# Kernel optimization log

Measured on AMD Instinct MI355X. Metric: run time of the kernel, lower is better.

## Reference

```python
import jax, jax.numpy as jnp
import numpy as np

EPS = 1e-5

def yat_dense(x, kernel, bias, alpha):
    # scaled by (sqrt(F)/log(1+F))**alpha, plus bias.
    y = x @ kernel  # [..., F]
    dist = jnp.sum(x * x, axis=-1, keepdims=True) + jnp.sum(kernel * kernel, axis=0) - 2.0 * y
    out = (y * y) / (dist + EPS)
    F = kernel.shape[1]
    scale = (jnp.sqrt(jnp.float32(F)) / jnp.log1p(jnp.float32(F))) ** alpha
    return out * scale + bias

def setup_inputs() -> dict:
    key = jax.random.key(0)
    ks = jax.random.split(key, 8)
    B, T, C = 8, 1024, 1024
    x = jax.random.normal(ks[0], (B, T, C), dtype=jnp.float32)
    mask = jnp.tril(jnp.ones((T, T), dtype=bool))[None, None, :, :]  # causal [1,1,T,T]
    W_attn = jax.random.normal(ks[1], (C, 3 * C), dtype=jnp.float32) * (C ** -0.5)
    b_attn = jnp.zeros((3 * C,), dtype=jnp.float32)
    alpha_attn = jnp.ones((1,), dtype=jnp.float32)
    W_proj = jax.random.normal(ks[2], (C, C), dtype=jnp.float32) * (C ** -0.5)
    b_proj = jnp.zeros((C,), dtype=jnp.float32)
    alpha_proj = jnp.ones((1,), dtype=jnp.float32)
    return {"x": x, "mask": mask, "W_attn": W_attn, "b_attn": b_attn,
            "alpha_attn": alpha_attn, "W_proj": W_proj, "b_proj": b_proj,
            "alpha_proj": alpha_proj}

def reference(x, mask, W_attn, b_attn, alpha_attn, W_proj, b_proj, alpha_proj):
    B, T, C = x.shape
    H = 16
    hd = C // H
    qkv = yat_dense(x, W_attn, b_attn, alpha_attn)           # [B,T,3C]
    qkv = qkv.reshape(B, T, 3 * H, hd)
    q, k, v = jnp.array_split(qkv, 3, axis=2)                # each [B,T,H,hd]
    scale = 1.0 / jnp.sqrt(jnp.float32(hd))
    attn = jnp.einsum('bqhd,bkhd->bhqk', q, k) * scale       # [B,H,T,T]
    attn = jnp.where(mask, attn, jnp.finfo(jnp.float32).min)
    attn = jax.nn.softmax(attn, axis=-1)
    out = jnp.einsum('bhqk,bkhd->bqhd', attn, v).reshape(B, T, C)
    out = yat_dense(out, W_proj, b_proj, alpha_proj)         # [B,T,C]
    return out
```

## Files before the change

### kernel.cpp

```cpp
#include <hip/hip_runtime.h>
#include <math.h>

#define EPS 1e-5f
#define QSCALE 0.18033688011f

typedef short s16x8 __attribute__((ext_vector_type(8)));
typedef float f32x4 __attribute__((ext_vector_type(4)));
typedef unsigned short ushort_t;
typedef unsigned int uint_t;

__device__ inline ushort_t f2bf(float f) {
  uint_t u = __float_as_uint(f);
  uint_t r = (u + 0x7fffu + ((u >> 16) & 1u)) >> 16;
  return (ushort_t)r;
}
__device__ inline float bf2f(ushort_t h) {
  return __uint_as_float(((uint_t)h) << 16);
}
__device__ inline uint_t cvtpk_bf16(float lo, float hi) {
  uint_t r;
  asm("v_cvt_pk_bf16_f32 %0, %1, %2" : "=v"(r) : "v"(lo), "v"(hi));
  return r;
}

__global__ __launch_bounds__(256) void cast_norm_k(const float* __restrict__ x,
                                                   ushort_t* __restrict__ xbf,
                                                   float* __restrict__ xnorm) {
  const int row = blockIdx.x * 4 + (threadIdx.x >> 6);
  const int lane = threadIdx.x & 63;
  const float4* p = (const float4*)(x + (size_t)row * 1024);
  ushort4* o = (ushort4*)(xbf + (size_t)row * 1024);
  float s = 0.f;
#pragma unroll
  for (int i = lane; i < 256; i += 64) {
    float4 v = p[i];
    s += v.x * v.x + v.y * v.y + v.z * v.z + v.w * v.w;
    o[i] = make_ushort4(f2bf(v.x), f2bf(v.y), f2bf(v.z), f2bf(v.w));
  }
#pragma unroll
  for (int off = 1; off < 64; off <<= 1) s += __shfl_xor(s, off, 64);
  if (lane == 0) xnorm[row] = s;
}

__global__ __launch_bounds__(256) void transpose_cast_k(
    const float* __restrict__ W, ushort_t* __restrict__ o, int K, int N) {
  __shared__ float t[32][33];
  const int n0 = blockIdx.x * 32, k0 = blockIdx.y * 32;
  const int tx = threadIdx.x & 31, ty = threadIdx.x >> 5;
#pragma unroll
  for (int j = 0; j < 4; ++j)
    t[ty + j * 8][tx] = W[(size_t)(k0 + ty + j * 8) * N + n0 + tx];
  __syncthreads();
#pragma unroll
  for (int j = 0; j < 4; ++j)
    o[(size_t)(n0 + ty + j * 8) * K + k0 + tx] = f2bf(t[tx][ty + j * 8]);
}

__global__ __launch_bounds__(256) void rownorm_bf16_k(const ushort_t* __restrict__ X,
                                                      float* __restrict__ out, int K) {
  const int row = blockIdx.x * 4 + (threadIdx.x >> 6);
  const int lane = threadIdx.x & 63;
  const ushort4* p = (const ushort4*)(X + (size_t)row * K);
  float s = 0.f;
  const int nq = K >> 2;
  for (int i = lane; i < nq; i += 64) {
    ushort4 v = p[i];
    float a = bf2f(v.x), b = bf2f(v.y), c = bf2f(v.z), d = bf2f(v.w);
    s += a * a + b * b + c * c + d * d;
  }
#pragma unroll
  for (int off = 1; off < 64; off <<= 1) s += __shfl_xor(s, off, 64);
  if (lane == 0) out[row] = s;
}

template <int MODE, int KK>
__global__ __launch_bounds__(256) void gemm_yat_mfma(
    const ushort_t* __restrict__ abf, const ushort_t* __restrict__ btbf,
    const float* __restrict__ bias, const float* __restrict__ alpha,
    const float* __restrict__ rown, const float* __restrict__ coln,
    void* __restrict__ outp, ushort_t* __restrict__ vtp, int M, int N) {
  __shared__ alignas(16) short lds[2 * 16384];

  const int tid = threadIdx.x;
  const int wid = tid >> 6;
  const int lane = tid & 63;
  const int g = lane >> 4;
  const int wm = wid >> 1, wn = wid & 1;

  const int nbx = gridDim.x;
  const int id = blockIdx.y * nbx + blockIdx.x;
  const int xcd = id & 7;
  const int sq = id >> 3;
  const int gq = sq >> 6;
  const int rr = sq & 63;
  const int bm = (xcd * 8 + (rr >> 3)) * 128;
  const int bn = (gq * 8 + (rr & 7)) * 128;

  f32x4 acc[4][4];
#pragma unroll
  for (int m = 0; m < 4; ++m)
#pragma unroll
    for (int n = 0; n < 4; ++n) acc[m][n] = (f32x4){0.f, 0.f, 0.f, 0.f};

  const int kc_sw = ((lane & 3) - ((lane >> 3) & 3)) & 3;
  const int slot_rd = (g + ((lane & 15) >> 1)) & 3;

  const ushort_t* srcb[8];
#pragma unroll
  for (int j = 0; j < 8; ++j) {
    const int q = wid + 4 * j;
    const int reg_idx = q >> 4;
    const int grp = (q >> 1) & 7;
    const int half = q & 1;
    const int grow = grp * 16 + (lane >> 2);
    const int gcol = half * 32 + kc_sw * 8;
    srcb[j] = (reg_idx == 0) ? abf + (size_t)(bm + grow) * KK + gcol
                             : btbf + (size_t)(bn + grow) * KK + gcol;
  }

  auto stage = [&](int buf, int t) {
#pragma unroll
    for (int j = 0; j < 8; ++j) {
      const int q = wid + 4 * j;
      const int reg_idx = q >> 4;
      const int grp = (q >> 1) & 7;
      const int half = q & 1;
      short* dst = &lds[buf * 16384 + reg_idx * 8192 + grp * 1024 + half * 512];
      __builtin_amdgcn_global_load_lds(
          (const __attribute__((address_space(1))) void*)(srcb[j] + t * 64),
          (__attribute__((address_space(3))) void*)dst, 16, 0, 0);
    }
  };

  stage(0, 0);
  __syncthreads();

  constexpr int NT = KK / 64;
#pragma unroll
  for (int t = 0; t < NT; ++t) {
    const int cur = t & 1;
    if (t + 1 < NT) stage(cur ^ 1, t + 1);

    s16x8 af[2][4], bfr[2][4];
#pragma unroll
    for (int kk = 0; kk < 2; ++kk) {
#pragma unroll
      for (int m = 0; m < 4; ++m) {
        const int off = cur * 16384 + (wm * 4 + m) * 1024 + kk * 512 +
                        (lane & 15) * 32 + slot_rd * 8;
        af[kk][m] = *(const s16x8*)&lds[off];
      }
#pragma unroll
      for (int n = 0; n < 4; ++n) {
        const int off = cur * 16384 + 8192 + (wn * 4 + n) * 1024 + kk * 512 +
                        (lane & 15) * 32 + slot_rd * 8;
        bfr[kk][n] = *(const s16x8*)&lds[off];
      }
    }
    __builtin_amdgcn_s_setprio(1);
#pragma unroll
    for (int kk = 0; kk < 2; ++kk)
#pragma unroll
      for (int m = 0; m < 4; ++m)
#pragma unroll
        for (int n = 0; n < 4; ++n)
          acc[m][n] = __builtin_amdgcn_mfma_f32_16x16x32_bf16(af[kk][m], bfr[kk][n],
                                                              acc[m][n], 0, 0, 0);
    __builtin_amdgcn_s_setprio(0);
    __syncthreads();
  }

  const float sc = powf(sqrtf((float)N) / log1pf((float)N), alpha[0]);
  const int r0 = (lane >> 4) * 4;
  const int c0 = lane & 15;
#pragma unroll
  for (int m = 0; m < 4; ++m) {
    const int rowb = bm + wm * 64 + m * 16 + r0;
    float rn[4] = {rown[rowb], rown[rowb + 1], rown[rowb + 2], rown[rowb + 3]};
#pragma unroll
    for (int n = 0; n < 4; ++n) {
      const int col = bn + wn * 64 + n * 16 + c0;
      const float cn = coln[col];
      const float bs = bias[col];
      f32x4 a = acc[m][n];
      float o4[4];
#pragma unroll
      for (int r = 0; r < 4; ++r) {
        const float y = a[r];
        const float dist = rn[r] + cn - 2.f * y + EPS;
        o4[r] = (y * y) / dist * sc + bs;
      }
      if (MODE == 1) {
        if (col < 1024) {
#pragma unroll
          for (int r = 0; r < 4; ++r) o4[r] *= QSCALE;
        }
        if (col >= 2048) {
          const int d = col & 63, hh = (col >> 6) & 15;
          const int bb = rowb >> 10, t0 = rowb & 1023;
          ushort4 pk = make_ushort4(f2bf(o4[0]), f2bf(o4[1]), f2bf(o4[2]), f2bf(o4[3]));
          *(ushort4*)(vtp + (((size_t)(bb * 16 + hh) * 64 + d) << 10) + t0) = pk;
        } else {
#pragma unroll
          for (int r = 0; r < 4; ++r)
            ((ushort_t*)outp)[(size_t)(rowb + r) * N + col] = f2bf(o4[r]);
        }
      } else {
#pragma unroll
        for (int r = 0; r < 4; ++r)
          ((float*)outp)[(size_t)(rowb + r) * N + col] = o4[r];
      }
    }
  }
}

__global__ __launch_bounds__(256) void attn_mfma_k(const ushort_t* __restrict__ qkv,
                                                   const ushort_t* __restrict__ vt,
                                                   ushort_t* __restrict__ out) {
  const int i = blockIdx.y * 8 + blockIdx.x;
  const int xcd = i & 7, s = i >> 3;
  const int bh = xcd * 16 + (s & 15);
  const int pairx = s >> 4;
  const int b = bh >> 4, h = bh & 15;

  const int tid = threadIdx.x;
  const int wid = tid >> 6;
  const int lane = tid & 63;
  const int g = lane >> 4;
  const int c = lane & 15;

  __shared__ alignas(16) ushort_t Ks[64][76];
  __shared__ alignas(16) ushort_t Vs[64][76];
  __shared__ alignas(16) ushort_t Pl[4][16][76];

  const int srow = tid >> 3;
  const int sd0 = (tid & 7) * 8;
  const ushort_t* kbase = qkv + (size_t)(b * 1024) * 3072 + 1024 + h * 64;
  const ushort_t* vbase = vt + ((size_t)(b * 16 + h) << 16);

#pragma unroll
  for (int pass = 0; pass < 2; ++pass) {
    const int qt = pass == 0 ? pairx : 15 - pairx;

    const ushort_t* qrow =
        qkv + ((size_t)(b * 1024 + qt * 64 + wid * 16 + c)) * 3072 + h * 64;
    s16x8 qf[2];
    qf[0] = *(const s16x8*)(qrow + g * 8);
    qf[1] = *(const s16x8*)(qrow + 32 + g * 8);

    f32x4 acc_o[4];
#pragma unroll
    for (int dt = 0; dt < 4; ++dt) acc_o[dt] = (f32x4){0.f, 0.f, 0.f, 0.f};
    float l_lane = 0.f;

    s16x8 kreg[2], vreg[2];
#pragma unroll
    for (int ii = 0; ii < 2; ++ii) {
      kreg[ii] = *(const s16x8*)(kbase + (size_t)(srow + ii * 32) * 3072 + sd0);
      vreg[ii] = *(const s16x8*)(vbase + (size_t)(srow + ii * 32) * 1024 + sd0);
    }

    for (int kt = 0; kt <= qt; ++kt) {
      __syncthreads();
#pragma unroll
      for (int ii = 0; ii < 2; ++ii) {
        *(s16x8*)&Ks[srow + ii * 32][sd0] = kreg[ii];
        *(s16x8*)&Vs[srow + ii * 32][sd0] = vreg[ii];
      }
      __syncthreads();

      if (kt < qt) {
#pragma unroll
        for (int ii = 0; ii < 2; ++ii) {
          kreg[ii] = *(const s16x8*)(kbase +
                                     (size_t)((kt + 1) * 64 + srow + ii * 32) * 3072 + sd0);
          vreg[ii] = *(const s16x8*)(vbase + (size_t)(srow + ii * 32) * 1024 +
                                     (kt + 1) * 64 + sd0);
        }
      }

      const bool diag = (kt == qt);
      const int jtmax = diag ? wid : 3;

      f32x4 sacc[4];
#pragma unroll
      for (int jt = 0; jt < 4; ++jt) sacc[jt] = (f32x4){0.f, 0.f, 0.f, 0.f};
      __builtin_amdgcn_s_setprio(1);
#pragma unroll
      for (int jt = 0; jt < 4; ++jt) {
        if (jt <= jtmax) {
          s16x8 kf0 = *(const s16x8*)&Ks[jt * 16 + c][g * 8];
          s16x8 kf1 = *(const s16x8*)&Ks[jt * 16 + c][32 + g * 8];
          sacc[jt] = __builtin_amdgcn_mfma_f32_16x16x32_bf16(kf0, qf[0], sacc[jt], 0, 0, 0);
          sacc[jt] = __builtin_amdgcn_mfma_f32_16x16x32_bf16(kf1, qf[1], sacc[jt], 0, 0, 0);
        }
      }
      __builtin_amdgcn_s_setprio(0);

      float p[4][4];
      float rs = 0.f;
#pragma unroll
      for (int jt = 0; jt < 4; ++jt)
#pragma unroll
        for (int r = 0; r < 4; ++r) {
          float v = sacc[jt][r];
          if (diag && (jt * 16 + g * 4 + r > wid * 16 + c)) v = -INFINITY;
          const float e = exp2f(v);
          p[jt][r] = e;
          rs += e;
        }
      l_lane += rs;

#pragma unroll
      for (int jt = 0; jt < 4; ++jt) {
        uint2 w;
        w.x = cvtpk_bf16(p[jt][0], p[jt][1]);
        w.y = cvtpk_bf16(p[jt][2], p[jt][3]);
        *(uint2*)&Pl[wid][c][jt * 16 + g * 4] = w;
      }

      const int kcmax = diag ? (wid >> 1) : 1;
      __builtin_amdgcn_s_setprio(1);
#pragma unroll
      for (int kc = 0; kc < 2; ++kc) {
        if (kc <= kcmax) {
          s16x8 pf = *(const s16x8*)&Pl[wid][c][kc * 32 + g * 8];
#pragma unroll
          for (int dt = 0; dt < 4; ++dt) {
            s16x8 vf = *(const s16x8*)&Vs[dt * 16 + c][kc * 32 + g * 8];
            acc_o[dt] = __builtin_amdgcn_mfma_f32_16x16x32_bf16(pf, vf, acc_o[dt], 0, 0, 0);
          }
        }
      }
      __builtin_amdgcn_s_setprio(0);
    }

    float lt = l_lane;
    lt += __shfl_xor(lt, 16, 64);
    lt += __shfl_xor(lt, 32, 64);

    float l_bc[4];
#pragma unroll
    for (int r = 0; r < 4; ++r) l_bc[r] = __shfl(lt, g * 4 + r, 16);
#pragma unroll
    for (int r = 0; r < 4; ++r) {
      const float inv = 1.f / l_bc[r];
      ushort_t* op =
          out + ((size_t)(b * 1024 + qt * 64 + wid * 16 + g * 4 + r)) * 1024 + h * 64 + c;
#pragma unroll
      for (int dt = 0; dt < 4; ++dt) op[dt * 16] = f2bf(acc_o[dt][r] * inv);
    }
  }
}

extern "C" void kernel_launch(void* const* d_in, const int* in_sizes, int n_in,
                              void* d_out, int out_size, void* d_ws, size_t ws_size,
                              hipStream_t stream) {
  const float* x = (const float*)d_in[0];
  const float* W_attn = (const float*)d_in[2];
  const float* b_attn = (const float*)d_in[3];
  const float* alpha_attn = (const float*)d_in[4];
  const float* W_proj = (const float*)d_in[5];
  const float* b_proj = (const float*)d_in[6];
  const float* alpha_proj = (const float*)d_in[7];
  float* out = (float*)d_out;

  char* ws = (char*)d_ws;
  ushort_t* qkv = (ushort_t*)(ws);
  ushort_t* attnout = (ushort_t*)(ws + 50331648ull);
  ushort_t* xbf = (ushort_t*)(ws + 67108864ull);
  ushort_t* watt = (ushort_t*)(ws + 83886080ull);
  ushort_t* wpjt = (ushort_t*)(ws + 90177536ull);
  float* xnorm = (float*)(ws + 92274688ull);
  float* anorm = (float*)(ws + 92307456ull);
  float* watn = (float*)(ws + 92340224ull);
  float* wpn = (float*)(ws + 92352512ull);
  ushort_t* vt = (ushort_t*)(ws + 92372992ull);

  const int M = 8192;

  cast_norm_k<<<M / 4, 256, 0, stream>>>(x, xbf, xnorm);
  transpose_cast_k<<<dim3(96, 32), 256, 0, stream>>>(W_attn, watt, 1024, 3072);
  transpose_cast_k<<<dim3(32, 32), 256, 0, stream>>>(W_proj, wpjt, 1024, 1024);
  rownorm_bf16_k<<<3072 / 4, 256, 0, stream>>>(watt, watn, 1024);
  rownorm_bf16_k<<<1024 / 4, 256, 0, stream>>>(wpjt, wpn, 1024);

  gemm_yat_mfma<1, 1024><<<dim3(3072 / 128, M / 128), 256, 0, stream>>>(
      xbf, watt, b_attn, alpha_attn, xnorm, watn, (void*)qkv, vt, M, 3072);

  attn_mfma_k<<<dim3(8, 128), 256, 0, stream>>>(qkv, vt, attnout);

  rownorm_bf16_k<<<M / 4, 256, 0, stream>>>(attnout, anorm, 1024);

  gemm_yat_mfma<0, 1024><<<dim3(1024 / 128, M / 128), 256, 0, stream>>>(
      attnout, wpjt, b_proj, alpha_proj, anorm, wpn, (void*)out, nullptr, M, 1024);
}
```

Before: 157.5 us.

## Fuse row-norm computations into producer kernels via atomic accumulation

Removes the three separate rownorm kernels. Weight column norms are now accumulated with atomics inside the transpose-cast kernel, and the attention output row norms inside the attention epilogue. The accumulators are zeroed in the cast kernel that runs first. This cuts three launches and one extra read of the 16MB attention output, at the cost of many float atomics and order-dependent summation.

```diff
diff --git a/kernel.cpp b/kernel.cpp
--- a/kernel.cpp
+++ b/kernel.cpp
@@ -25,7 +25,15 @@
 
 __global__ __launch_bounds__(256) void cast_norm_k(const float* __restrict__ x,
                                                    ushort_t* __restrict__ xbf,
-                                                   float* __restrict__ xnorm) {
+                                                   float* __restrict__ xnorm,
+                                                   float* __restrict__ anorm,
+                                                   float* __restrict__ watn,
+                                                   float* __restrict__ wpn) {
+  const int gid = blockIdx.x * 256 + threadIdx.x;
+  if (gid < 8192) anorm[gid] = 0.f;
+  if (gid < 3072) watn[gid] = 0.f;
+  if (gid < 1024) wpn[gid] = 0.f;
+
   const int row = blockIdx.x * 4 + (threadIdx.x >> 6);
   const int lane = threadIdx.x & 63;
   const float4* p = (const float4*)(x + (size_t)row * 1024);
@@ -42,8 +50,9 @@
   if (lane == 0) xnorm[row] = s;
 }
 
-__global__ __launch_bounds__(256) void transpose_cast_k(
-    const float* __restrict__ W, ushort_t* __restrict__ o, int K, int N) {
+__global__ __launch_bounds__(256) void transpose_cast_norm_k(
+    const float* __restrict__ W, ushort_t* __restrict__ o,
+    float* __restrict__ cnorm, int K, int N) {
   __shared__ float t[32][33];
   const int n0 = blockIdx.x * 32, k0 = blockIdx.y * 32;
   const int tx = threadIdx.x & 31, ty = threadIdx.x >> 5;
@@ -52,25 +61,15 @@
     t[ty + j * 8][tx] = W[(size_t)(k0 + ty + j * 8) * N + n0 + tx];
   __syncthreads();
 #pragma unroll
-  for (int j = 0; j < 4; ++j)
-    o[(size_t)(n0 + ty + j * 8) * K + k0 + tx] = f2bf(t[tx][ty + j * 8]);
-}
-
-__global__ __launch_bounds__(256) void rownorm_bf16_k(const ushort_t* __restrict__ X,
-                                                      float* __restrict__ out, int K) {
-  const int row = blockIdx.x * 4 + (threadIdx.x >> 6);
-  const int lane = threadIdx.x & 63;
-  const ushort4* p = (const ushort4*)(X + (size_t)row * K);
-  float s = 0.f;
-  const int nq = K >> 2;
-  for (int i = lane; i < nq; i += 64) {
-    ushort4 v = p[i];
-    float a = bf2f(v.x), b = bf2f(v.y), c = bf2f(v.z), d = bf2f(v.w);
-    s += a * a + b * b + c * c + d * d;
-  }
-#pragma unroll
-  for (int off = 1; off < 64; off <<= 1) s += __shfl_xor(s, off, 64);
-  if (lane == 0) out[row] = s;
+  for (int j = 0; j < 4; ++j) {
+    const ushort_t h = f2bf(t[tx][ty + j * 8]);
+    o[(size_t)(n0 + ty + j * 8) * K + k0 + tx] = h;
+    const float v = bf2f(h);
+    float s = v * v;
+#pragma unroll
+    for (int off = 1; off < 32; off <<= 1) s += __shfl_xor(s, off, 32);
+    if (tx == 0) atomicAdd(cnorm + n0 + ty + j * 8, s);
+  }
 }
 
 template <int MODE, int KK>
@@ -216,7 +215,8 @@
 
 __global__ __launch_bounds__(256) void attn_mfma_k(const ushort_t* __restrict__ qkv,
                                                    const ushort_t* __restrict__ vt,
-                                                   ushort_t* __restrict__ out) {
+                                                   ushort_t* __restrict__ out,
+                                                   float* __restrict__ anorm) {
   const int i = blockIdx.y * 8 + blockIdx.x;
   const int xcd = i & 7, s = i >> 3;
   const int bh = xcd * 16 + (s & 15);
@@ -345,10 +345,21 @@
 #pragma unroll
     for (int r = 0; r < 4; ++r) {
       const float inv = 1.f / l_bc[r];
-      ushort_t* op =
-          out + ((size_t)(b * 1024 + qt * 64 + wid * 16 + g * 4 + r)) * 1024 + h * 64 + c;
-#pragma unroll
-      for (int dt = 0; dt < 4; ++dt) op[dt * 16] = f2bf(acc_o[dt][r] * inv);
+      const int rowg = b * 1024 + qt * 64 + wid * 16 + g * 4 + r;
+      ushort_t* op = out + (size_t)rowg * 1024 + h * 64 + c;
+      float ns = 0.f;
+#pragma unroll
+      for (int dt = 0; dt < 4; ++dt) {
+        const ushort_t ob = f2bf(acc_o[dt][r] * inv);
+        op[dt * 16] = ob;
+        const float of = bf2f(ob);
+        ns += of * of;
+      }
+      ns += __shfl_xor(ns, 1, 16);
+      ns += __shfl_xor(ns, 2, 16);
+      ns += __shfl_xor(ns, 4, 16);
+      ns += __shfl_xor(ns, 8, 16);
+      if (c == 0) atomicAdd(anorm + (rowg & 8191), ns);
     }
   }
 }
@@ -379,18 +390,14 @@
 
   const int M = 8192;
 
-  cast_norm_k<<<M / 4, 256, 0, stream>>>(x, xbf, xnorm);
-  transpose_cast_k<<<dim3(96, 32), 256, 0, stream>>>(W_attn, watt, 1024, 3072);
-  transpose_cast_k<<<dim3(32, 32), 256, 0, stream>>>(W_proj, wpjt, 1024, 1024);
-  rownorm_bf16_k<<<3072 / 4, 256, 0, stream>>>(watt, watn, 1024);
-  rownorm_bf16_k<<<1024 / 4, 256, 0, stream>>>(wpjt, wpn, 1024);
+  cast_norm_k<<<M / 4, 256, 0, stream>>>(x, xbf, xnorm, anorm, watn, wpn);
+  transpose_cast_norm_k<<<dim3(96, 32), 256, 0, stream>>>(W_attn, watt, watn, 1024, 3072);
+  transpose_cast_norm_k<<<dim3(32, 32), 256, 0, stream>>>(W_proj, wpjt, wpn, 1024, 1024);
 
   gemm_yat_mfma<1, 1024><<<dim3(3072 / 128, M / 128), 256, 0, stream>>>(
       xbf, watt, b_attn, alpha_attn, xnorm, watn, (void*)qkv, vt, M, 3072);
 
-  attn_mfma_k<<<dim3(8, 128), 256, 0, stream>>>(qkv, vt, attnout);
-
-  rownorm_bf16_k<<<M / 4, 256, 0, stream>>>(attnout, anorm, 1024);
+  attn_mfma_k<<<dim3(8, 128), 256, 0, stream>>>(qkv, vt, attnout, anorm);
 
   gemm_yat_mfma<0, 1024><<<dim3(1024 / 128, M / 128), 256, 0, stream>>>(
       attnout, wpjt, b_proj, alpha_proj, anorm, wpn, (void*)out, nullptr, M, 1024);
```

Measured after the change: 163.2 us. 3.6% more time.

## Merge paired causal query tiles into one K/V sweep sharing loaded tiles

Applied to the files above, without the earlier changes.

The attention kernel used to make two sequential passes, one per query tile of a balanced pair (qt and 15-qt), and reloaded the K/V tiles from global memory in each pass. It now holds both query tiles' fragments and accumulators at once and makes a single sweep over key tiles up to the larger qt. Each K/V tile staged in LDS serves the long tile and, while kt <= qtA, the short tile too. This removes the duplicate global loads and barriers of the shorter pass, at the cost of more live registers (two accumulator sets and two Q fragment sets), which may reduce occupancy.

```diff
diff --git a/kernel.cpp b/kernel.cpp
--- a/kernel.cpp
+++ b/kernel.cpp
@@ -222,6 +222,8 @@
   const int bh = xcd * 16 + (s & 15);
   const int pairx = s >> 4;
   const int b = bh >> 4, h = bh & 15;
+  const int qtA = pairx;
+  const int qtB = 15 - pairx;
 
   const int tid = threadIdx.x;
   const int wid = tid >> 6;
@@ -238,50 +240,53 @@
   const ushort_t* kbase = qkv + (size_t)(b * 1024) * 3072 + 1024 + h * 64;
   const ushort_t* vbase = vt + ((size_t)(b * 16 + h) << 16);
 
-#pragma unroll
-  for (int pass = 0; pass < 2; ++pass) {
-    const int qt = pass == 0 ? pairx : 15 - pairx;
-
-    const ushort_t* qrow =
-        qkv + ((size_t)(b * 1024 + qt * 64 + wid * 16 + c)) * 3072 + h * 64;
-    s16x8 qf[2];
-    qf[0] = *(const s16x8*)(qrow + g * 8);
-    qf[1] = *(const s16x8*)(qrow + 32 + g * 8);
-
-    f32x4 acc_o[4];
-#pragma unroll
-    for (int dt = 0; dt < 4; ++dt) acc_o[dt] = (f32x4){0.f, 0.f, 0.f, 0.f};
-    float l_lane = 0.f;
-
-    s16x8 kreg[2], vreg[2];
+  const ushort_t* qrowA =
+      qkv + ((size_t)(b * 1024 + qtA * 64 + wid * 16 + c)) * 3072 + h * 64;
+  const ushort_t* qrowB =
+      qkv + ((size_t)(b * 1024 + qtB * 64 + wid * 16 + c)) * 3072 + h * 64;
+  s16x8 qfA[2], qfB[2];
+  qfA[0] = *(const s16x8*)(qrowA + g * 8);
+  qfA[1] = *(const s16x8*)(qrowA + 32 + g * 8);
+  qfB[0] = *(const s16x8*)(qrowB + g * 8);
+  qfB[1] = *(const s16x8*)(qrowB + 32 + g * 8);
+
+  f32x4 accA[4], accB[4];
+#pragma unroll
+  for (int dt = 0; dt < 4; ++dt) {
+    accA[dt] = (f32x4){0.f, 0.f, 0.f, 0.f};
+    accB[dt] = (f32x4){0.f, 0.f, 0.f, 0.f};
+  }
+  float lA = 0.f, lB = 0.f;
+
+  s16x8 kreg[2], vreg[2];
+#pragma unroll
+  for (int ii = 0; ii < 2; ++ii) {
+    kreg[ii] = *(const s16x8*)(kbase + (size_t)(srow + ii * 32) * 3072 + sd0);
+    vreg[ii] = *(const s16x8*)(vbase + (size_t)(srow + ii * 32) * 1024 + sd0);
+  }
+
+  for (int kt = 0; kt <= qtB; ++kt) {
+    __syncthreads();
 #pragma unroll
     for (int ii = 0; ii < 2; ++ii) {
-      kreg[ii] = *(const s16x8*)(kbase + (size_t)(srow + ii * 32) * 3072 + sd0);
-      vreg[ii] = *(const s16x8*)(vbase + (size_t)(srow + ii * 32) * 1024 + sd0);
-    }
-
-    for (int kt = 0; kt <= qt; ++kt) {
-      __syncthreads();
+      *(s16x8*)&Ks[srow + ii * 32][sd0] = kreg[ii];
+      *(s16x8*)&Vs[srow + ii * 32][sd0] = vreg[ii];
+    }
+    __syncthreads();
+
+    if (kt < qtB) {
 #pragma unroll
       for (int ii = 0; ii < 2; ++ii) {
-        *(s16x8*)&Ks[srow + ii * 32][sd0] = kreg[ii];
-        *(s16x8*)&Vs[srow + ii * 32][sd0] = vreg[ii];
-      }
-      __syncthreads();
-
-      if (kt < qt) {
-#pragma unroll
-        for (int ii = 0; ii < 2; ++ii) {
-          kreg[ii] = *(const s16x8*)(kbase +
-                                     (size_t)((kt + 1) * 64 + srow + ii * 32) * 3072 + sd0);
-          vreg[ii] = *(const s16x8*)(vbase + (size_t)(srow + ii * 32) * 1024 +
-                                     (kt + 1) * 64 + sd0);
-        }
-      }
-
-      const bool diag = (kt == qt);
+        kreg[ii] = *(const s16x8*)(kbase +
+                                   (size_t)((kt + 1) * 64 + srow + ii * 32) * 3072 + sd0);
+        vreg[ii] = *(const s16x8*)(vbase + (size_t)(srow + ii * 32) * 1024 +
+                                   (kt + 1) * 64 + sd0);
+      }
+    }
+
+    {
+      const bool diag = (kt == qtB);
       const int jtmax = diag ? wid : 3;
-
       f32x4 sacc[4];
 #pragma unroll
       for (int jt = 0; jt < 4; ++jt) sacc[jt] = (f32x4){0.f, 0.f, 0.f, 0.f};
@@ -291,8 +296,8 @@
         if (jt <= jtmax) {
           s16x8 kf0 = *(const s16x8*)&Ks[jt * 16 + c][g * 8];
           s16x8 kf1 = *(const s16x8*)&Ks[jt * 16 + c][32 + g * 8];
-          sacc[jt] = __builtin_amdgcn_mfma_f32_16x16x32_bf16(kf0, qf[0], sacc[jt], 0, 0, 0);
-          sacc[jt] = __builtin_amdgcn_mfma_f32_16x16x32_bf16(kf1, qf[1], sacc[jt], 0, 0, 0);
+          sacc[jt] = __builtin_amdgcn_mfma_f32_16x16x32_bf16(kf0, qfB[0], sacc[jt], 0, 0, 0);
+          sacc[jt] = __builtin_amdgcn_mfma_f32_16x16x32_bf16(kf1, qfB[1], sacc[jt], 0, 0, 0);
         }
       }
       __builtin_amdgcn_s_setprio(0);
@@ -309,7 +314,7 @@
           p[jt][r] = e;
           rs += e;
         }
-      l_lane += rs;
+      lB += rs;
 
 #pragma unroll
       for (int jt = 0; jt < 4; ++jt) {
@@ -328,17 +333,77 @@
 #pragma unroll
           for (int dt = 0; dt < 4; ++dt) {
             s16x8 vf = *(const s16x8*)&Vs[dt * 16 + c][kc * 32 + g * 8];
-            acc_o[dt] = __builtin_amdgcn_mfma_f32_16x16x32_bf16(pf, vf, acc_o[dt], 0, 0, 0);
+            accB[dt] = __builtin_amdgcn_mfma_f32_16x16x32_bf16(pf, vf, accB[dt], 0, 0, 0);
           }
         }
       }
       __builtin_amdgcn_s_setprio(0);
     }
 
-    float lt = l_lane;
+    if (kt <= qtA) {
+      const bool diag = (kt == qtA);
+      const int jtmax = diag ? wid : 3;
+      f32x4 sacc[4];
+#pragma unroll
+      for (int jt = 0; jt < 4; ++jt) sacc[jt] = (f32x4){0.f, 0.f, 0.f, 0.f};
+      __builtin_amdgcn_s_setprio(1);
+#pragma unroll
+      for (int jt = 0; jt < 4; ++jt) {
+        if (jt <= jtmax) {
+          s16x8 kf0 = *(const s16x8*)&Ks[jt * 16 + c][g * 8];
+          s16x8 kf1 = *(const s16x8*)&Ks[jt * 16 + c][32 + g * 8];
+          sacc[jt] = __builtin_amdgcn_mfma_f32_16x16x32_bf16(kf0, qfA[0], sacc[jt], 0, 0, 0);
+          sacc[jt] = __builtin_amdgcn_mfma_f32_16x16x32_bf16(kf1, qfA[1], sacc[jt], 0, 0, 0);
+        }
+      }
+      __builtin_amdgcn_s_setprio(0);
+
+      float p[4][4];
+      float rs = 0.f;
+#pragma unroll
+      for (int jt = 0; jt < 4; ++jt)
+#pragma unroll
+        for (int r = 0; r < 4; ++r) {
+          float v = sacc[jt][r];
+          if (diag && (jt * 16 + g * 4 + r > wid * 16 + c)) v = -INFINITY;
+          const float e = exp2f(v);
+          p[jt][r] = e;
+          rs += e;
+        }
+      lA += rs;
+
+#pragma unroll
+      for (int jt = 0; jt < 4; ++jt) {
+        uint2 w;
+        w.x = cvtpk_bf16(p[jt][0], p[jt][1]);
+        w.y = cvtpk_bf16(p[jt][2], p[jt][3]);
+        *(uint2*)&Pl[wid][c][jt * 16 + g * 4] = w;
+      }
+
+      const int kcmax = diag ? (wid >> 1) : 1;
+      __builtin_amdgcn_s_setprio(1);
+#pragma unroll
+      for (int kc = 0; kc < 2; ++kc) {
+        if (kc <= kcmax) {
+          s16x8 pf = *(const s16x8*)&Pl[wid][c][kc * 32 + g * 8];
+#pragma unroll
+          for (int dt = 0; dt < 4; ++dt) {
+            s16x8 vf = *(const s16x8*)&Vs[dt * 16 + c][kc * 32 + g * 8];
+            accA[dt] = __builtin_amdgcn_mfma_f32_16x16x32_bf16(pf, vf, accA[dt], 0, 0, 0);
+          }
+        }
+      }
+      __builtin_amdgcn_s_setprio(0);
+    }
+  }
+
+#pragma unroll
+  for (int tsel = 0; tsel < 2; ++tsel) {
+    const int qt = tsel == 0 ? qtA : qtB;
+    float lt = tsel == 0 ? lA : lB;
+    const f32x4* ac = tsel == 0 ? accA : accB;
     lt += __shfl_xor(lt, 16, 64);
     lt += __shfl_xor(lt, 32, 64);
-
     float l_bc[4];
 #pragma unroll
     for (int r = 0; r < 4; ++r) l_bc[r] = __shfl(lt, g * 4 + r, 16);
@@ -348,7 +413,7 @@
       ushort_t* op =
           out + ((size_t)(b * 1024 + qt * 64 + wid * 16 + g * 4 + r)) * 1024 + h * 64 + c;
 #pragma unroll
-      for (int dt = 0; dt < 4; ++dt) op[dt * 16] = f2bf(acc_o[dt][r] * inv);
+      for (int dt = 0; dt < 4; ++dt) op[dt * 16] = f2bf(ac[dt][r] * inv);
     }
   }
 }
```

Measured after the change: 163.6 us. +3.9%, slower.
